# Performance work log

Hardware: AMD Instinct MI355X
Metric: run time of the kernel (lower is better)

Reference implementation:

```python
import jax, jax.numpy as jnp
import numpy as np

B, S, L, F = 32, 48, 64, 256


def setup_inputs() -> dict:
    key = jax.random.key(0)
    ks = jax.random.split(key, 7)
    return {
        "features": jax.random.normal(ks[0], (B, S, L, F), dtype=jnp.float32),
        "src_locs": jax.random.normal(ks[1], (B, L, 2), dtype=jnp.float32),
        "tar_locs": jax.random.normal(ks[2], (B, 2), dtype=jnp.float32),
        "W1": jax.random.normal(ks[3], (F, F), dtype=jnp.float32) * (1.0 / np.sqrt(F)),
        "b1": jax.random.normal(ks[4], (F,), dtype=jnp.float32) * 0.02,
        "W2": jax.random.normal(ks[5], (F, 1), dtype=jnp.float32) * (1.0 / np.sqrt(F)),
        "b2": jax.random.normal(ks[6], (1,), dtype=jnp.float32) * 0.02,
    }


def reference(features, src_locs, tar_locs, W1, b1, W2, b2):
    # features: (B, S, L, F); src_locs: (B, L, 2); tar_locs: (B, 2)
    # MLP score: Linear(F,F) + ReLU + Linear(F,1) + ReLU -> (B, S, L, 1)
    attn = jax.nn.relu(jnp.einsum('bslf,fg->bslg', features, W1) + b1)
    attn = jax.nn.relu(jnp.einsum('bslf,fo->bslo', attn, W2) + b2)  # (B,S,L,1)
    # inverse-distance weights over stations: (B, L)
    dists = jnp.sqrt(jnp.sum((src_locs - tar_locs[:, None, :]) ** 2, axis=-1))
    inv_dists = 1.0 / dists  # (B, L)
    # broadcast to (B, 1, L, 1), softmax over src_length axis (axis=2)
    attn_scores = jax.nn.softmax(attn * inv_dists[:, None, :, None], axis=2)
    # weighted sum over stations -> (B, S, F)
    return jnp.sum(features * attn_scores, axis=2)
```

## Files before the change

kernel.cpp:

```cpp
#include <hip/hip_runtime.h>
#include <hip/hip_fp16.h>
#include <math.h>

typedef _Float16 half8 __attribute__((ext_vector_type(8)));
typedef float floatx4 __attribute__((ext_vector_type(4)));

#define BB 32
#define SS 48
#define LL 64
#define FF 256

__global__ __launch_bounds__(256) void prep_w(const float* __restrict__ W1,
                                              _Float16* __restrict__ whi,
                                              _Float16* __restrict__ wlo) {
    int idx = blockIdx.x * 256 + threadIdx.x;
    int j    = idx & 7;
    int lane = (idx >> 3) & 63;
    int nt   = (idx >> 9) & 15;
    int kt   = idx >> 13;
    int k = kt * 32 + ((lane >> 4) & 3) * 8 + j;
    int n = nt * 16 + (lane & 15);
    float x = W1[k * FF + n];
    _Float16 hi = (_Float16)x;
    _Float16 lo = (_Float16)(x - (float)hi);
    whi[idx] = hi;
    wlo[idx] = lo;
}

__global__ __launch_bounds__(256, 2) void ida_mfma(
    const float* __restrict__ features,
    const float* __restrict__ src_locs,
    const float* __restrict__ tar_locs,
    const _Float16* __restrict__ whi,
    const _Float16* __restrict__ wlo,
    const float* __restrict__ b1,
    const float* __restrict__ W2,
    const float* __restrict__ b2,
    float* __restrict__ out)
{
    __shared__ _Float16 Ahi[8192];
    __shared__ _Float16 Alo[8192];
    __shared__ float SP[LL * 4];
    __shared__ float wbuf[LL];
    __shared__ float red[4 * FF];

    const int t    = threadIdx.x;
    const int w    = t >> 6;
    const int lane = t & 63;
    const int quad = lane >> 4;
    const int l16  = lane & 15;
    const int bs   = blockIdx.x;
    const int b    = bs / SS;

    const float* Xg = features + (size_t)bs * (LL * FF);

    floatx4 acc[4][4] = {};
    half8 bh[4][4], bl[4][4];

    #pragma unroll
    for (int ktl = 0; ktl < 4; ++ktl)
        #pragma unroll
        for (int nt = 0; nt < 4; ++nt) {
            size_t off = ((size_t)(ktl * 16 + w * 4 + nt) * 64 + lane) * 8;
            bh[ktl][nt] = *((const half8*)(whi + off));
            bl[ktl][nt] = *((const half8*)(wlo + off));
        }

    for (int ktl = 0; ktl < 4; ++ktl) {
        const float4* p = (const float4*)(Xg + (w * 16 + l16) * FF + ktl * 32 + quad * 8);
        float4 x0 = p[0], x1 = p[1];
        float xs[8] = {x0.x, x0.y, x0.z, x0.w, x1.x, x1.y, x1.z, x1.w};
        half8 hi, lo;
        #pragma unroll
        for (int j = 0; j < 8; ++j) {
            _Float16 h = (_Float16)xs[j];
            hi[j] = h;
            lo[j] = (_Float16)(xs[j] - (float)h);
        }
        *((half8*)&Ahi[((w * 4 + ktl) * 64 + lane) * 8]) = hi;
        *((half8*)&Alo[((w * 4 + ktl) * 64 + lane) * 8]) = lo;
    }

    float4 a1raw[8];
    #pragma unroll
    for (int ktl = 0; ktl < 4; ++ktl) {
        const float4* p = (const float4*)(Xg + (w * 16 + l16) * FF + (4 + ktl) * 32 + quad * 8);
        a1raw[2 * ktl + 0] = p[0];
        a1raw[2 * ktl + 1] = p[1];
    }

    __syncthreads();

    #pragma unroll
    for (int ktl = 0; ktl < 4; ++ktl) {
        #pragma unroll
        for (int mt = 0; mt < 4; ++mt) {
            half8 ahi = *((half8*)&Ahi[((mt * 4 + ktl) * 64 + lane) * 8]);
            half8 alo = *((half8*)&Alo[((mt * 4 + ktl) * 64 + lane) * 8]);
            #pragma unroll
            for (int nt = 0; nt < 4; ++nt) {
                acc[mt][nt] = __builtin_amdgcn_mfma_f32_16x16x32_f16(ahi, bh[ktl][nt], acc[mt][nt], 0, 0, 0);
                acc[mt][nt] = __builtin_amdgcn_mfma_f32_16x16x32_f16(ahi, bl[ktl][nt], acc[mt][nt], 0, 0, 0);
                acc[mt][nt] = __builtin_amdgcn_mfma_f32_16x16x32_f16(alo, bh[ktl][nt], acc[mt][nt], 0, 0, 0);
            }
        }
    }

    #pragma unroll
    for (int ktl = 0; ktl < 4; ++ktl)
        #pragma unroll
        for (int nt = 0; nt < 4; ++nt) {
            size_t off = ((size_t)((4 + ktl) * 16 + w * 4 + nt) * 64 + lane) * 8;
            bh[ktl][nt] = *((const half8*)(whi + off));
            bl[ktl][nt] = *((const half8*)(wlo + off));
        }

    __syncthreads();

    for (int ktl = 0; ktl < 4; ++ktl) {
        float4 x0 = a1raw[2 * ktl + 0], x1 = a1raw[2 * ktl + 1];
        float xs[8] = {x0.x, x0.y, x0.z, x0.w, x1.x, x1.y, x1.z, x1.w};
        half8 hi, lo;
        #pragma unroll
        for (int j = 0; j < 8; ++j) {
            _Float16 h = (_Float16)xs[j];
            hi[j] = h;
            lo[j] = (_Float16)(xs[j] - (float)h);
        }
        *((half8*)&Ahi[((w * 4 + ktl) * 64 + lane) * 8]) = hi;
        *((half8*)&Alo[((w * 4 + ktl) * 64 + lane) * 8]) = lo;
    }
    __syncthreads();

    #pragma unroll
    for (int ktl = 0; ktl < 4; ++ktl) {
        #pragma unroll
        for (int mt = 0; mt < 4; ++mt) {
            half8 ahi = *((half8*)&Ahi[((mt * 4 + ktl) * 64 + lane) * 8]);
            half8 alo = *((half8*)&Alo[((mt * 4 + ktl) * 64 + lane) * 8]);
            #pragma unroll
            for (int nt = 0; nt < 4; ++nt) {
                acc[mt][nt] = __builtin_amdgcn_mfma_f32_16x16x32_f16(ahi, bh[ktl][nt], acc[mt][nt], 0, 0, 0);
                acc[mt][nt] = __builtin_amdgcn_mfma_f32_16x16x32_f16(ahi, bl[ktl][nt], acc[mt][nt], 0, 0, 0);
                acc[mt][nt] = __builtin_amdgcn_mfma_f32_16x16x32_f16(alo, bh[ktl][nt], acc[mt][nt], 0, 0, 0);
            }
        }
    }

    float b1v[4], w2v[4];
    #pragma unroll
    for (int nt = 0; nt < 4; ++nt) {
        int n = (w * 4 + nt) * 16 + l16;
        b1v[nt] = b1[n];
        w2v[nt] = W2[n];
    }
    #pragma unroll
    for (int mt = 0; mt < 4; ++mt) {
        #pragma unroll
        for (int r = 0; r < 4; ++r) {
            float p = 0.f;
            #pragma unroll
            for (int nt = 0; nt < 4; ++nt) {
                float h = fmaxf(acc[mt][nt][r] + b1v[nt], 0.f);
                p = fmaf(h, w2v[nt], p);
            }
            p += __shfl_xor(p, 1);
            p += __shfl_xor(p, 2);
            p += __shfl_xor(p, 4);
            p += __shfl_xor(p, 8);
            if (l16 == 0) SP[(mt * 16 + quad * 4 + r) * 4 + w] = p;
        }
    }
    __syncthreads();

    if (t < LL) {
        float s = SP[4 * t] + SP[4 * t + 1] + SP[4 * t + 2] + SP[4 * t + 3] + b2[0];
        float score = fmaxf(s, 0.f);
        float dx = src_locs[(b * LL + t) * 2 + 0] - tar_locs[b * 2 + 0];
        float dy = src_locs[(b * LL + t) * 2 + 1] - tar_locs[b * 2 + 1];
        float inv = 1.0f / sqrtf(dx * dx + dy * dy);
        float logit = score * inv;
        float m = logit;
        #pragma unroll
        for (int o = 32; o > 0; o >>= 1) m = fmaxf(m, __shfl_xor(m, o));
        float e = __expf(logit - m);
        float se = e;
        #pragma unroll
        for (int o = 32; o > 0; o >>= 1) se += __shfl_xor(se, o);
        wbuf[t] = e / se;
    }
    __syncthreads();

    {
        const float4* Xg4 = (const float4*)Xg;
        floatx4 o = {0.f, 0.f, 0.f, 0.f};
        #pragma unroll
        for (int lr = 0; lr < 16; ++lr) {
            int l = w * 16 + lr;
            float wl = wbuf[l];
            float4 x = Xg4[l * 64 + lane];
            o[0] = fmaf(x.x, wl, o[0]);
            o[1] = fmaf(x.y, wl, o[1]);
            o[2] = fmaf(x.z, wl, o[2]);
            o[3] = fmaf(x.w, wl, o[3]);
        }
        #pragma unroll
        for (int j = 0; j < 4; ++j)
            red[w * FF + lane * 4 + j] = o[j];
    }
    __syncthreads();
    {
        float o = red[0 * FF + t] + red[1 * FF + t] + red[2 * FF + t] + red[3 * FF + t];
        out[(size_t)bs * FF + t] = o;
    }
}

extern "C" void kernel_launch(void* const* d_in, const int* in_sizes, int n_in,
                              void* d_out, int out_size, void* d_ws, size_t ws_size,
                              hipStream_t stream) {
    const float* features = (const float*)d_in[0];
    const float* src_locs = (const float*)d_in[1];
    const float* tar_locs = (const float*)d_in[2];
    const float* W1       = (const float*)d_in[3];
    const float* b1       = (const float*)d_in[4];
    const float* W2       = (const float*)d_in[5];
    const float* b2       = (const float*)d_in[6];
    float* out = (float*)d_out;

    _Float16* whi = (_Float16*)d_ws;
    _Float16* wlo = whi + FF * FF;

    prep_w<<<dim3(FF * FF / 256), dim3(256), 0, stream>>>(W1, whi, wlo);
    ida_mfma<<<dim3(BB * SS), dim3(256), 0, stream>>>(
        features, src_locs, tar_locs, whi, wlo, b1, W2, b2, out);
}
```

Baseline: 182.5 us.

## Use 512-thread blocks with 8 waves splitting N and streaming W1 fragments

The kernel goes from 4 to 8 waves per block. Each wave now owns 2 N-tiles instead of 4, which halves the accumulator and B-fragment register footprint. Instead of preloading all 16 W1 hi/lo fragments per half, it double-buffers them one k-step ahead. The intent is higher occupancy and better latency hiding on the MFMA and global-load path. The cost is more global/L2 traffic for W1 fragments, larger shared reduction buffers, and an 8-way reduction at the end.

```diff
diff --git a/kernel.cpp b/kernel.cpp
--- a/kernel.cpp
+++ b/kernel.cpp
@@ -27,7 +27,7 @@
     wlo[idx] = lo;
 }
 
-__global__ __launch_bounds__(256, 2) void ida_mfma(
+__global__ __launch_bounds__(512, 4) void ida_mfma(
     const float* __restrict__ features,
     const float* __restrict__ src_locs,
     const float* __restrict__ tar_locs,
@@ -40,9 +40,9 @@
 {
     __shared__ _Float16 Ahi[8192];
     __shared__ _Float16 Alo[8192];
-    __shared__ float SP[LL * 4];
+    __shared__ float SP[LL * 8];
     __shared__ float wbuf[LL];
-    __shared__ float red[4 * FF];
+    __shared__ float red[8 * FF];
 
     const int t    = threadIdx.x;
     const int w    = t >> 6;
@@ -54,20 +54,15 @@
 
     const float* Xg = features + (size_t)bs * (LL * FF);
 
-    floatx4 acc[4][4] = {};
-    half8 bh[4][4], bl[4][4];
-
-    #pragma unroll
-    for (int ktl = 0; ktl < 4; ++ktl)
-        #pragma unroll
-        for (int nt = 0; nt < 4; ++nt) {
-            size_t off = ((size_t)(ktl * 16 + w * 4 + nt) * 64 + lane) * 8;
-            bh[ktl][nt] = *((const half8*)(whi + off));
-            bl[ktl][nt] = *((const half8*)(wlo + off));
-        }
-
-    for (int ktl = 0; ktl < 4; ++ktl) {
-        const float4* p = (const float4*)(Xg + (w * 16 + l16) * FF + ktl * 32 + quad * 8);
+    floatx4 acc[4][2] = {};
+    half8 bh[2], bl[2], nbh[2], nbl[2];
+
+    #pragma unroll
+    for (int it = 0; it < 2; ++it) {
+        int g   = it * 8 + w;
+        int row = (g >> 2) * 16 + l16;
+        int kc  = (g & 3) * 32 + quad * 8;
+        const float4* p = (const float4*)(Xg + row * FF + kc);
         float4 x0 = p[0], x1 = p[1];
         float xs[8] = {x0.x, x0.y, x0.z, x0.w, x1.x, x1.y, x1.z, x1.w};
         half8 hi, lo;
@@ -77,48 +72,73 @@
             hi[j] = h;
             lo[j] = (_Float16)(xs[j] - (float)h);
         }
-        *((half8*)&Ahi[((w * 4 + ktl) * 64 + lane) * 8]) = hi;
-        *((half8*)&Alo[((w * 4 + ktl) * 64 + lane) * 8]) = lo;
-    }
-
-    float4 a1raw[8];
-    #pragma unroll
-    for (int ktl = 0; ktl < 4; ++ktl) {
-        const float4* p = (const float4*)(Xg + (w * 16 + l16) * FF + (4 + ktl) * 32 + quad * 8);
-        a1raw[2 * ktl + 0] = p[0];
-        a1raw[2 * ktl + 1] = p[1];
-    }
-
-    __syncthreads();
-
-    #pragma unroll
-    for (int ktl = 0; ktl < 4; ++ktl) {
-        #pragma unroll
-        for (int mt = 0; mt < 4; ++mt) {
-            half8 ahi = *((half8*)&Ahi[((mt * 4 + ktl) * 64 + lane) * 8]);
-            half8 alo = *((half8*)&Alo[((mt * 4 + ktl) * 64 + lane) * 8]);
-            #pragma unroll
-            for (int nt = 0; nt < 4; ++nt) {
-                acc[mt][nt] = __builtin_amdgcn_mfma_f32_16x16x32_f16(ahi, bh[ktl][nt], acc[mt][nt], 0, 0, 0);
-                acc[mt][nt] = __builtin_amdgcn_mfma_f32_16x16x32_f16(ahi, bl[ktl][nt], acc[mt][nt], 0, 0, 0);
-                acc[mt][nt] = __builtin_amdgcn_mfma_f32_16x16x32_f16(alo, bh[ktl][nt], acc[mt][nt], 0, 0, 0);
-            }
-        }
-    }
-
-    #pragma unroll
-    for (int ktl = 0; ktl < 4; ++ktl)
-        #pragma unroll
-        for (int nt = 0; nt < 4; ++nt) {
-            size_t off = ((size_t)((4 + ktl) * 16 + w * 4 + nt) * 64 + lane) * 8;
-            bh[ktl][nt] = *((const half8*)(whi + off));
-            bl[ktl][nt] = *((const half8*)(wlo + off));
-        }
-
-    __syncthreads();
-
-    for (int ktl = 0; ktl < 4; ++ktl) {
-        float4 x0 = a1raw[2 * ktl + 0], x1 = a1raw[2 * ktl + 1];
+        *((half8*)&Ahi[(g * 64 + lane) * 8]) = hi;
+        *((half8*)&Alo[(g * 64 + lane) * 8]) = lo;
+    }
+
+    float4 a1raw[4];
+    #pragma unroll
+    for (int it = 0; it < 2; ++it) {
+        int g   = it * 8 + w;
+        int row = (g >> 2) * 16 + l16;
+        int kc  = (g & 3) * 32 + quad * 8;
+        const float4* p = (const float4*)(Xg + row * FF + 128 + kc);
+        a1raw[2 * it + 0] = p[0];
+        a1raw[2 * it + 1] = p[1];
+    }
+
+    #pragma unroll
+    for (int ntl = 0; ntl < 2; ++ntl) {
+        size_t off = ((size_t)(0 * 16 + (w * 2 + ntl)) * 64 + lane) * 8;
+        bh[ntl] = *((const half8*)(whi + off));
+        bl[ntl] = *((const half8*)(wlo + off));
+    }
+
+    __syncthreads();
+
+#define COMPUTE_HALF(h)                                                          \
+    _Pragma("unroll")                                                            \
+    for (int ktl = 0; ktl < 4; ++ktl) {                                          \
+        if (ktl < 3) {                                                           \
+            _Pragma("unroll")                                                    \
+            for (int ntl = 0; ntl < 2; ++ntl) {                                  \
+                size_t off = ((size_t)(((h) * 4 + ktl + 1) * 16 + (w * 2 + ntl)) * 64 + lane) * 8; \
+                nbh[ntl] = *((const half8*)(whi + off));                         \
+                nbl[ntl] = *((const half8*)(wlo + off));                         \
+            }                                                                    \
+        }                                                                        \
+        _Pragma("unroll")                                                        \
+        for (int mt = 0; mt < 4; ++mt) {                                         \
+            half8 ahi = *((half8*)&Ahi[((mt * 4 + ktl) * 64 + lane) * 8]);       \
+            half8 alo = *((half8*)&Alo[((mt * 4 + ktl) * 64 + lane) * 8]);       \
+            _Pragma("unroll")                                                    \
+            for (int ntl = 0; ntl < 2; ++ntl) {                                  \
+                acc[mt][ntl] = __builtin_amdgcn_mfma_f32_16x16x32_f16(ahi, bh[ntl], acc[mt][ntl], 0, 0, 0); \
+                acc[mt][ntl] = __builtin_amdgcn_mfma_f32_16x16x32_f16(ahi, bl[ntl], acc[mt][ntl], 0, 0, 0); \
+                acc[mt][ntl] = __builtin_amdgcn_mfma_f32_16x16x32_f16(alo, bh[ntl], acc[mt][ntl], 0, 0, 0); \
+            }                                                                    \
+        }                                                                        \
+        if (ktl < 3) {                                                           \
+            bh[0] = nbh[0]; bh[1] = nbh[1];                                      \
+            bl[0] = nbl[0]; bl[1] = nbl[1];                                      \
+        }                                                                        \
+    }
+
+    COMPUTE_HALF(0)
+
+    #pragma unroll
+    for (int ntl = 0; ntl < 2; ++ntl) {
+        size_t off = ((size_t)(4 * 16 + (w * 2 + ntl)) * 64 + lane) * 8;
+        bh[ntl] = *((const half8*)(whi + off));
+        bl[ntl] = *((const half8*)(wlo + off));
+    }
+
+    __syncthreads();
+
+    #pragma unroll
+    for (int it = 0; it < 2; ++it) {
+        int g = it * 8 + w;
+        float4 x0 = a1raw[2 * it + 0], x1 = a1raw[2 * it + 1];
         float xs[8] = {x0.x, x0.y, x0.z, x0.w, x1.x, x1.y, x1.z, x1.w};
         half8 hi, lo;
         #pragma unroll
@@ -127,32 +147,20 @@
             hi[j] = h;
             lo[j] = (_Float16)(xs[j] - (float)h);
         }
-        *((half8*)&Ahi[((w * 4 + ktl) * 64 + lane) * 8]) = hi;
-        *((half8*)&Alo[((w * 4 + ktl) * 64 + lane) * 8]) = lo;
-    }
-    __syncthreads();
-
-    #pragma unroll
-    for (int ktl = 0; ktl < 4; ++ktl) {
-        #pragma unroll
-        for (int mt = 0; mt < 4; ++mt) {
-            half8 ahi = *((half8*)&Ahi[((mt * 4 + ktl) * 64 + lane) * 8]);
-            half8 alo = *((half8*)&Alo[((mt * 4 + ktl) * 64 + lane) * 8]);
-            #pragma unroll
-            for (int nt = 0; nt < 4; ++nt) {
-                acc[mt][nt] = __builtin_amdgcn_mfma_f32_16x16x32_f16(ahi, bh[ktl][nt], acc[mt][nt], 0, 0, 0);
-                acc[mt][nt] = __builtin_amdgcn_mfma_f32_16x16x32_f16(ahi, bl[ktl][nt], acc[mt][nt], 0, 0, 0);
-                acc[mt][nt] = __builtin_amdgcn_mfma_f32_16x16x32_f16(alo, bh[ktl][nt], acc[mt][nt], 0, 0, 0);
-            }
-        }
-    }
-
-    float b1v[4], w2v[4];
-    #pragma unroll
-    for (int nt = 0; nt < 4; ++nt) {
-        int n = (w * 4 + nt) * 16 + l16;
-        b1v[nt] = b1[n];
-        w2v[nt] = W2[n];
+        *((half8*)&Ahi[(g * 64 + lane) * 8]) = hi;
+        *((half8*)&Alo[(g * 64 + lane) * 8]) = lo;
+    }
+    __syncthreads();
+
+    COMPUTE_HALF(1)
+#undef COMPUTE_HALF
+
+    float b1v[2], w2v[2];
+    #pragma unroll
+    for (int ntl = 0; ntl < 2; ++ntl) {
+        int n = (w * 2 + ntl) * 16 + l16;
+        b1v[ntl] = b1[n];
+        w2v[ntl] = W2[n];
     }
     #pragma unroll
     for (int mt = 0; mt < 4; ++mt) {
@@ -160,21 +168,22 @@
         for (int r = 0; r < 4; ++r) {
             float p = 0.f;
             #pragma unroll
-            for (int nt = 0; nt < 4; ++nt) {
-                float h = fmaxf(acc[mt][nt][r] + b1v[nt], 0.f);
-                p = fmaf(h, w2v[nt], p);
+            for (int ntl = 0; ntl < 2; ++ntl) {
+                float h = fmaxf(acc[mt][ntl][r] + b1v[ntl], 0.f);
+                p = fmaf(h, w2v[ntl], p);
             }
             p += __shfl_xor(p, 1);
             p += __shfl_xor(p, 2);
             p += __shfl_xor(p, 4);
             p += __shfl_xor(p, 8);
-            if (l16 == 0) SP[(mt * 16 + quad * 4 + r) * 4 + w] = p;
+            if (l16 == 0) SP[(mt * 16 + quad * 4 + r) * 8 + w] = p;
         }
     }
     __syncthreads();
 
     if (t < LL) {
-        float s = SP[4 * t] + SP[4 * t + 1] + SP[4 * t + 2] + SP[4 * t + 3] + b2[0];
+        float s = SP[8 * t + 0] + SP[8 * t + 1] + SP[8 * t + 2] + SP[8 * t + 3]
+                + SP[8 * t + 4] + SP[8 * t + 5] + SP[8 * t + 6] + SP[8 * t + 7] + b2[0];
         float score = fmaxf(s, 0.f);
         float dx = src_locs[(b * LL + t) * 2 + 0] - tar_locs[b * 2 + 0];
         float dy = src_locs[(b * LL + t) * 2 + 1] - tar_locs[b * 2 + 1];
@@ -195,8 +204,8 @@
         const float4* Xg4 = (const float4*)Xg;
         floatx4 o = {0.f, 0.f, 0.f, 0.f};
         #pragma unroll
-        for (int lr = 0; lr < 16; ++lr) {
-            int l = w * 16 + lr;
+        for (int lr = 0; lr < 8; ++lr) {
+            int l = w * 8 + lr;
             float wl = wbuf[l];
             float4 x = Xg4[l * 64 + lane];
             o[0] = fmaf(x.x, wl, o[0]);
@@ -204,13 +213,12 @@
             o[2] = fmaf(x.z, wl, o[2]);
             o[3] = fmaf(x.w, wl, o[3]);
         }
-        #pragma unroll
-        for (int j = 0; j < 4; ++j)
-            red[w * FF + lane * 4 + j] = o[j];
-    }
-    __syncthreads();
-    {
-        float o = red[0 * FF + t] + red[1 * FF + t] + red[2 * FF + t] + red[3 * FF + t];
+        *((floatx4*)&red[w * FF + lane * 4]) = o;
+    }
+    __syncthreads();
+    if (t < FF) {
+        float o = red[0 * FF + t] + red[1 * FF + t] + red[2 * FF + t] + red[3 * FF + t]
+                + red[4 * FF + t] + red[5 * FF + t] + red[6 * FF + t] + red[7 * FF + t];
         out[(size_t)bs * FF + t] = o;
     }
 }
@@ -231,6 +239,6 @@
     _Float16* wlo = whi + FF * FF;
 
     prep_w<<<dim3(FF * FF / 256), dim3(256), 0, stream>>>(W1, whi, wlo);
-    ida_mfma<<<dim3(BB * SS), dim3(256), 0, stream>>>(
+    ida_mfma<<<dim3(BB * SS), dim3(512), 0, stream>>>(
         features, src_locs, tar_locs, whi, wlo, b1, W2, b2, out);
 }
```

New measurement: 190.5 us. 4.4% more time.

## Give each wave full N range with register-resident A and double-buffered B stream

Applied to the files above, without the earlier changes.

Each wave now owns 16 full rows of the feature tile and computes all 256 output columns. The hi/lo A fragments stay in registers, so the LDS staging buffers and several block barriers go away. W1 fragments are streamed from global memory with a double-buffered prefetch, and the per-row score reduction no longer needs a cross-wave step. Each wave also computes the softmax redundantly and broadcasts weights with shuffles, and the feature rows for the weighted sum are prefetched before the softmax. The cost is much higher register pressure (acc[16], ahi/alo[8], xraw[16]), which could cut occupancy, and each wave now reads the whole of W1 rather than a quarter of it.

```diff
diff --git a/kernel.cpp b/kernel.cpp
--- a/kernel.cpp
+++ b/kernel.cpp
@@ -38,14 +38,11 @@
     const float* __restrict__ b2,
     float* __restrict__ out)
 {
-    __shared__ _Float16 Ahi[8192];
-    __shared__ _Float16 Alo[8192];
-    __shared__ float SP[LL * 4];
-    __shared__ float wbuf[LL];
-    __shared__ float red[4 * FF];
+    __shared__ float SP[LL];
+    __shared__ float red[4][FF];
 
     const int t    = threadIdx.x;
-    const int w    = t >> 6;
+    const int wv   = t >> 6;
     const int lane = t & 63;
     const int quad = lane >> 4;
     const int l16  = lane & 15;
@@ -54,164 +51,128 @@
 
     const float* Xg = features + (size_t)bs * (LL * FF);
 
-    floatx4 acc[4][4] = {};
-    half8 bh[4][4], bl[4][4];
+    float4 araw[16];
+    const float* Arow = Xg + (wv * 16 + l16) * FF;
+    #pragma unroll
+    for (int kt = 0; kt < 8; ++kt) {
+        const float4* p = (const float4*)(Arow + kt * 32 + quad * 8);
+        araw[2 * kt + 0] = p[0];
+        araw[2 * kt + 1] = p[1];
+    }
 
+    half8 cbh[2][4], cbl[2][4];
     #pragma unroll
-    for (int ktl = 0; ktl < 4; ++ktl)
-        #pragma unroll
-        for (int nt = 0; nt < 4; ++nt) {
-            size_t off = ((size_t)(ktl * 16 + w * 4 + nt) * 64 + lane) * 8;
-            bh[ktl][nt] = *((const half8*)(whi + off));
-            bl[ktl][nt] = *((const half8*)(wlo + off));
-        }
+    for (int k2 = 0; k2 < 4; ++k2) {
+        size_t off = ((size_t)(k2 * 16 + 0) * 64 + lane) * 8;
+        cbh[0][k2] = *((const half8*)(whi + off));
+        cbl[0][k2] = *((const half8*)(wlo + off));
+    }
 
-    for (int ktl = 0; ktl < 4; ++ktl) {
-        const float4* p = (const float4*)(Xg + (w * 16 + l16) * FF + ktl * 32 + quad * 8);
-        float4 x0 = p[0], x1 = p[1];
-        float xs[8] = {x0.x, x0.y, x0.z, x0.w, x1.x, x1.y, x1.z, x1.w};
-        half8 hi, lo;
+    float dx = src_locs[(b * LL + lane) * 2 + 0] - tar_locs[b * 2 + 0];
+    float dy = src_locs[(b * LL + lane) * 2 + 1] - tar_locs[b * 2 + 1];
+    float inv_d = 1.0f / sqrtf(dx * dx + dy * dy);
+    float b2v = b2[0];
+
+    half8 ahi[8], alo[8];
+    #pragma unroll
+    for (int kt = 0; kt < 8; ++kt) {
+        float xs[8] = {araw[2 * kt].x,     araw[2 * kt].y,     araw[2 * kt].z,     araw[2 * kt].w,
+                       araw[2 * kt + 1].x, araw[2 * kt + 1].y, araw[2 * kt + 1].z, araw[2 * kt + 1].w};
         #pragma unroll
         for (int j = 0; j < 8; ++j) {
             _Float16 h = (_Float16)xs[j];
-            hi[j] = h;
-            lo[j] = (_Float16)(xs[j] - (float)h);
-        }
-        *((half8*)&Ahi[((w * 4 + ktl) * 64 + lane) * 8]) = hi;
-        *((half8*)&Alo[((w * 4 + ktl) * 64 + lane) * 8]) = lo;
-    }
-
-    float4 a1raw[8];
-    #pragma unroll
-    for (int ktl = 0; ktl < 4; ++ktl) {
-        const float4* p = (const float4*)(Xg + (w * 16 + l16) * FF + (4 + ktl) * 32 + quad * 8);
-        a1raw[2 * ktl + 0] = p[0];
-        a1raw[2 * ktl + 1] = p[1];
-    }
-
-    __syncthreads();
-
-    #pragma unroll
-    for (int ktl = 0; ktl < 4; ++ktl) {
-        #pragma unroll
-        for (int mt = 0; mt < 4; ++mt) {
-            half8 ahi = *((half8*)&Ahi[((mt * 4 + ktl) * 64 + lane) * 8]);
-            half8 alo = *((half8*)&Alo[((mt * 4 + ktl) * 64 + lane) * 8]);
-            #pragma unroll
-            for (int nt = 0; nt < 4; ++nt) {
-                acc[mt][nt] = __builtin_amdgcn_mfma_f32_16x16x32_f16(ahi, bh[ktl][nt], acc[mt][nt], 0, 0, 0);
-                acc[mt][nt] = __builtin_amdgcn_mfma_f32_16x16x32_f16(ahi, bl[ktl][nt], acc[mt][nt], 0, 0, 0);
-                acc[mt][nt] = __builtin_amdgcn_mfma_f32_16x16x32_f16(alo, bh[ktl][nt], acc[mt][nt], 0, 0, 0);
-            }
+            ahi[kt][j] = h;
+            alo[kt][j] = (_Float16)(xs[j] - (float)h);
         }
     }
 
+    floatx4 acc[16] = {};
+    float b1v[16], w2v[16];
+
     #pragma unroll
-    for (int ktl = 0; ktl < 4; ++ktl)
+    for (int i = 0; i < 32; ++i) {
+        const int p   = i >> 2;
+        const int q   = i & 3;
+        const int nt  = 2 * p + (q & 1);
+        const int kh  = q >> 1;
+        const int cur = i & 1;
+        if (i < 31) {
+            const int i2  = i + 1;
+            const int p2  = i2 >> 2, q2 = i2 & 3;
+            const int nt2 = 2 * p2 + (q2 & 1);
+            const int kh2 = q2 >> 1;
+            #pragma unroll
+            for (int k2 = 0; k2 < 4; ++k2) {
+                size_t off = ((size_t)((kh2 * 4 + k2) * 16 + nt2) * 64 + lane) * 8;
+                cbh[cur ^ 1][k2] = *((const half8*)(whi + off));
+                cbl[cur ^ 1][k2] = *((const half8*)(wlo + off));
+            }
+        } else {
+            #pragma unroll
+            for (int n2 = 0; n2 < 16; ++n2) {
+                b1v[n2] = b1[n2 * 16 + l16];
+                w2v[n2] = W2[n2 * 16 + l16];
+            }
+        }
         #pragma unroll
-        for (int nt = 0; nt < 4; ++nt) {
-            size_t off = ((size_t)((4 + ktl) * 16 + w * 4 + nt) * 64 + lane) * 8;
-            bh[ktl][nt] = *((const half8*)(whi + off));
-            bl[ktl][nt] = *((const half8*)(wlo + off));
+        for (int k2 = 0; k2 < 4; ++k2) {
+            const int kt = kh * 4 + k2;
+            acc[nt] = __builtin_amdgcn_mfma_f32_16x16x32_f16(ahi[kt], cbh[cur][k2], acc[nt], 0, 0, 0);
+            acc[nt] = __builtin_amdgcn_mfma_f32_16x16x32_f16(ahi[kt], cbl[cur][k2], acc[nt], 0, 0, 0);
+            acc[nt] = __builtin_amdgcn_mfma_f32_16x16x32_f16(alo[kt], cbh[cur][k2], acc[nt], 0, 0, 0);
         }
+    }
 
-    __syncthreads();
+    float4 xraw[16];
+    const float4* Xg4 = (const float4*)Xg;
+    #pragma unroll
+    for (int lr = 0; lr < 16; ++lr)
+        xraw[lr] = Xg4[(wv * 16 + lr) * 64 + lane];
 
-    for (int ktl = 0; ktl < 4; ++ktl) {
-        float4 x0 = a1raw[2 * ktl + 0], x1 = a1raw[2 * ktl + 1];
-        float xs[8] = {x0.x, x0.y, x0.z, x0.w, x1.x, x1.y, x1.z, x1.w};
-        half8 hi, lo;
+    #pragma unroll
+    for (int r = 0; r < 4; ++r) {
+        float pr = 0.f;
         #pragma unroll
-        for (int j = 0; j < 8; ++j) {
-            _Float16 h = (_Float16)xs[j];
-            hi[j] = h;
-            lo[j] = (_Float16)(xs[j] - (float)h);
+        for (int nt = 0; nt < 16; ++nt) {
+            float h = fmaxf(acc[nt][r] + b1v[nt], 0.f);
+            pr = fmaf(h, w2v[nt], pr);
         }
-        *((half8*)&Ahi[((w * 4 + ktl) * 64 + lane) * 8]) = hi;
-        *((half8*)&Alo[((w * 4 + ktl) * 64 + lane) * 8]) = lo;
+        pr += __shfl_xor(pr, 1);
+        pr += __shfl_xor(pr, 2);
+        pr += __shfl_xor(pr, 4);
+        pr += __shfl_xor(pr, 8);
+        if (l16 == 0) SP[wv * 16 + quad * 4 + r] = pr;
     }
     __syncthreads();
 
+    float s = SP[lane] + b2v;
+    float score = fmaxf(s, 0.f);
+    float logit = score * inv_d;
+    float m = logit;
     #pragma unroll
-    for (int ktl = 0; ktl < 4; ++ktl) {
-        #pragma unroll
-        for (int mt = 0; mt < 4; ++mt) {
-            half8 ahi = *((half8*)&Ahi[((mt * 4 + ktl) * 64 + lane) * 8]);
-            half8 alo = *((half8*)&Alo[((mt * 4 + ktl) * 64 + lane) * 8]);
-            #pragma unroll
-            for (int nt = 0; nt < 4; ++nt) {
-                acc[mt][nt] = __builtin_amdgcn_mfma_f32_16x16x32_f16(ahi, bh[ktl][nt], acc[mt][nt], 0, 0, 0);
-                acc[mt][nt] = __builtin_amdgcn_mfma_f32_16x16x32_f16(ahi, bl[ktl][nt], acc[mt][nt], 0, 0, 0);
-                acc[mt][nt] = __builtin_amdgcn_mfma_f32_16x16x32_f16(alo, bh[ktl][nt], acc[mt][nt], 0, 0, 0);
-            }
-        }
-    }
-
-    float b1v[4], w2v[4];
+    for (int o = 32; o > 0; o >>= 1) m = fmaxf(m, __shfl_xor(m, o));
+    float e = __expf(logit - m);
+    float se = e;
     #pragma unroll
-    for (int nt = 0; nt < 4; ++nt) {
-        int n = (w * 4 + nt) * 16 + l16;
-        b1v[nt] = b1[n];
-        w2v[nt] = W2[n];
-    }
-    #pragma unroll
-    for (int mt = 0; mt < 4; ++mt) {
-        #pragma unroll
-        for (int r = 0; r < 4; ++r) {
-            float p = 0.f;
-            #pragma unroll
-            for (int nt = 0; nt < 4; ++nt) {
-                float h = fmaxf(acc[mt][nt][r] + b1v[nt], 0.f);
-                p = fmaf(h, w2v[nt], p);
-            }
-            p += __shfl_xor(p, 1);
-            p += __shfl_xor(p, 2);
-            p += __shfl_xor(p, 4);
-            p += __shfl_xor(p, 8);
-            if (l16 == 0) SP[(mt * 16 + quad * 4 + r) * 4 + w] = p;
-        }
-    }
-    __syncthreads();
-
-    if (t < LL) {
-        float s = SP[4 * t] + SP[4 * t + 1] + SP[4 * t + 2] + SP[4 * t + 3] + b2[0];
-        float score = fmaxf(s, 0.f);
-        float dx = src_locs[(b * LL + t) * 2 + 0] - tar_locs[b * 2 + 0];
-        float dy = src_locs[(b * LL + t) * 2 + 1] - tar_locs[b * 2 + 1];
-        float inv = 1.0f / sqrtf(dx * dx + dy * dy);
-        float logit = score * inv;
-        float m = logit;
-        #pragma unroll
-        for (int o = 32; o > 0; o >>= 1) m = fmaxf(m, __shfl_xor(m, o));
-        float e = __expf(logit - m);
-        float se = e;
-        #pragma unroll
-        for (int o = 32; o > 0; o >>= 1) se += __shfl_xor(se, o);
-        wbuf[t] = e / se;
-    }
-    __syncthreads();
+    for (int o = 32; o > 0; o >>= 1) se += __shfl_xor(se, o);
+    float wgt = e / se;
 
     {
-        const float4* Xg4 = (const float4*)Xg;
-        floatx4 o = {0.f, 0.f, 0.f, 0.f};
+        floatx4 o4 = {0.f, 0.f, 0.f, 0.f};
         #pragma unroll
         for (int lr = 0; lr < 16; ++lr) {
-            int l = w * 16 + lr;
-            float wl = wbuf[l];
-            float4 x = Xg4[l * 64 + lane];
-            o[0] = fmaf(x.x, wl, o[0]);
-            o[1] = fmaf(x.y, wl, o[1]);
-            o[2] = fmaf(x.z, wl, o[2]);
-            o[3] = fmaf(x.w, wl, o[3]);
+            float wl = __shfl(wgt, wv * 16 + lr);
+            o4[0] = fmaf(xraw[lr].x, wl, o4[0]);
+            o4[1] = fmaf(xraw[lr].y, wl, o4[1]);
+            o4[2] = fmaf(xraw[lr].z, wl, o4[2]);
+            o4[3] = fmaf(xraw[lr].w, wl, o4[3]);
         }
-        #pragma unroll
-        for (int j = 0; j < 4; ++j)
-            red[w * FF + lane * 4 + j] = o[j];
+        *((floatx4*)&red[wv][lane * 4]) = o4;
     }
     __syncthreads();
     {
-        float o = red[0 * FF + t] + red[1 * FF + t] + red[2 * FF + t] + red[3 * FF + t];
-        out[(size_t)bs * FF + t] = o;
+        float oo = red[0][t] + red[1][t] + red[2][t] + red[3][t];
+        out[(size_t)bs * FF + t] = oo;
     }
 }
 
```

Measured after the change: 234.2 us. 28.3% more time.
